# Kernel tuning notes

Measured on AMD Instinct MI355X. Metric: run time of the kernel, lower is better.

Reference implementation:

```python
import jax, jax.numpy as jnp
import numpy as np

N = 4096          # num_nodes
B = 16            # num_graphs (equal-sized contiguous segments)
L = 2             # max degree -> (L+1)**2 = 9 spherical components
NUM_DEG = (L + 1) ** 2
F = 128           # input feature dim
FQK = 128         # query/key feature dim
FV = 128          # value feature dim
MAX_FREQ = 8.0
MAX_LEN = 10.0

# degree index of each spherical component: [0, 1,1,1, 2,2,2,2,2]
DEG_IDX = np.array([l for l in range(L + 1) for _ in range(2 * l + 1)], dtype=np.int32)
# Lebedev grid num=6: octahedron vertices, equal weights 1/6
GRID_U = np.array([[1, 0, 0], [-1, 0, 0], [0, 1, 0], [0, -1, 0], [0, 0, 1], [0, 0, -1]], dtype=np.float32)
GRID_W = np.full((6,), 1.0 / 6.0, dtype=np.float32)


def _edense(x, W, b, deg_idx):
    y = jnp.einsum('npmf,mfg->npmg', x, W[deg_idx])
    return y.at[:, :, 0, :].add(b)


def _erope(x, cos, sin):
    # x: (N, 1, M9, Fqk); cos/sin: (N, G, H) with H = Fqk // 2
    x1 = x[:, None, :, :, 0::2]  # (N,1,1,M9,H) -> broadcast over G
    x2 = x[:, None, :, :, 1::2]
    c = cos[:, :, None, None, :]
    s = sin[:, :, None, None, :]
    r1 = x1 * c - x2 * s
    r2 = x1 * s + x2 * c
    out = jnp.stack([r1, r2], axis=-1)  # interleave pairs back
    return out.reshape(out.shape[:-2] + (-1,))  # (N, G, 1, M9, Fqk)


def setup_inputs() -> dict:
    key = jax.random.key(0)
    ks = jax.random.split(key, 8)
    inputs = jax.random.normal(ks[0], (N, 1, NUM_DEG, F), jnp.float32)
    positions = jax.random.normal(ks[1], (N, 3), jnp.float32) * 3.0
    # contiguous equal-sized graph segments (jraph-style padding convention)
    batch_segments = jnp.repeat(jnp.arange(B), N // B)
    graph_mask = jnp.ones((B,), bool)
    s = 1.0 / np.sqrt(F)
    Wq = jax.random.normal(ks[2], (L + 1, F, FQK), jnp.float32) * s
    Wk = jax.random.normal(ks[3], (L + 1, F, FQK), jnp.float32) * s
    Wv = jax.random.normal(ks[4], (L + 1, F, FV), jnp.float32) * s
    bq = jnp.zeros((FQK,), jnp.float32)
    bk = jnp.zeros((FQK,), jnp.float32)
    bv = jnp.zeros((FV,), jnp.float32)
    return dict(inputs=inputs, positions=positions, batch_segments=batch_segments,
                graph_mask=graph_mask, Wq=Wq, bq=bq, Wk=Wk, bk=bk, Wv=Wv, bv=bv)


def reference(inputs, positions, batch_segments, graph_mask, Wq, bq, Wk, bk, Wv, bv):
    deg_idx = jnp.asarray(DEG_IDX)
    grid_u = jnp.asarray(GRID_U)
    grid_w = jnp.asarray(GRID_W)
    G = grid_u.shape[0]
    # frequencies per frequency_init_fn: linspace(0, max_freq, Fqk/2) / max_length
    theta = jnp.linspace(0.0, MAX_FREQ, FQK // 2, dtype=jnp.float32) / MAX_LEN  # (H,)

    q = _edense(inputs, Wq, bq, deg_idx)  # (N,1,M9,FQK)
    k = _edense(inputs, Wk, bk, deg_idx)
    v = _edense(inputs, Wv, bv, deg_idx)  # (N,1,M9,FV)

    # Euclidean RoPE phases: angle[n,g,h] = (pos_n . u_g) * theta_h
    phase = positions @ grid_u.T           # (N,G)
    ang = phase[:, :, None] * theta        # (N,G,H)
    cos, sin = jnp.cos(ang), jnp.sin(ang)

    Mdim = NUM_DEG * FQK
    Ddim = NUM_DEG * FV
    qr = _erope(q, cos, sin).reshape(N, G, Mdim)  # (N,G,M)
    kr = _erope(k, cos, sin).reshape(N, G, Mdim)
    vf = v.reshape(N, Ddim)

    # per-graph linear attention with Lebedev quadrature (contiguous equal segments)
    n = N // B
    qr_b = qr.reshape(B, n, G, Mdim)
    kr_b = kr.reshape(B, n, G, Mdim)
    v_b = vf.reshape(B, n, Ddim)
    kv = jnp.einsum('bngm,bnd->bgmd', kr_b, v_b)          # KV summaries
    kv = kv * grid_w[None, :, None, None]                 # quadrature weights
    out = jnp.einsum('bngm,bgmd->bnd', qr_b, kv)          # integrate over grid
    out = out.reshape(N, 1, NUM_DEG, FV)
    mask = graph_mask[batch_segments]                     # (N,)
    return jnp.where(mask[:, None, None, None], out, 0.0)
```

## Files before the change

### kernel.cpp

```cpp
#include <hip/hip_runtime.h>


typedef unsigned short u16;
typedef __attribute__((ext_vector_type(8))) short short8;
typedef __attribute__((ext_vector_type(4))) float f32x4;

static constexpr int N_NODES = 4096;
static constexpr int NBATCH  = 16;
static constexpr int NB      = 256;
static constexpr int NDEG    = 9;
static constexpr int MD      = NDEG * 128;
static constexpr int KTOT    = 6 * MD;
static constexpr size_t ASLICE = (size_t)NBATCH * NB * NB;

static constexpr size_t OFF_WT  = 0;
static constexpr size_t OFF_QR  = OFF_WT  + (size_t)9*16384*2;
static constexpr size_t OFF_KR  = OFF_QR  + (size_t)N_NODES*KTOT*2;
static constexpr size_t OFF_VT  = OFF_KR  + (size_t)N_NODES*KTOT*2;
static constexpr size_t OFF_AP  = OFF_VT  + (size_t)N_NODES*MD*2;

__device__ inline u16 f2bf(float x) {
    union { float f; unsigned u; } v; v.f = x;
    unsigned r = v.u + 0x7fffu + ((v.u >> 16) & 1u);
    return (u16)(r >> 16);
}
__device__ inline float bf2f(u16 h) {
    union { unsigned u; float f; } v; v.u = ((unsigned)h) << 16; return v.f;
}
__device__ inline unsigned pk2bf(float a, float b) {
#if __has_builtin(__builtin_amdgcn_cvt_pk_bf16_f32)
    typedef __attribute__((ext_vector_type(2))) __bf16 bf2_t;
    union { bf2_t v; unsigned u; } cv;
    cv.v = __builtin_amdgcn_cvt_pk_bf16_f32(a, b);
    return cv.u;
#else
    return (unsigned)f2bf(a) | ((unsigned)f2bf(b) << 16);
#endif
}

__global__ __launch_bounds__(256) void k_prep(const float* __restrict__ Wq,
                                              const float* __restrict__ Wk,
                                              const float* __restrict__ Wv,
                                              u16* __restrict__ wt) {
    int t = blockIdx.x, tid = threadIdx.x;
    int blk = t >> 2, tt = t & 3;
    int mat = blk / 3, l = blk % 3;
    const float* W = (mat == 0 ? Wq : (mat == 1 ? Wk : Wv)) + (size_t)l * 16384;
    int j0 = (tt >> 1) * 64, f0 = (tt & 1) * 64;
    __shared__ u16 tile[64 * 72];
    for (int e = tid; e < 1024; e += 256) {
        int r = e >> 4, c = e & 15;
        float4 wv = *(const float4*)(W + (size_t)(f0 + r) * 128 + j0 + c * 4);
        tile[(c * 4 + 0) * 72 + r] = f2bf(wv.x);
        tile[(c * 4 + 1) * 72 + r] = f2bf(wv.y);
        tile[(c * 4 + 2) * 72 + r] = f2bf(wv.z);
        tile[(c * 4 + 3) * 72 + r] = f2bf(wv.w);
    }
    __syncthreads();
    u16* dst = wt + (size_t)blk * 16384;
    for (int e = tid; e < 512; e += 256) {
        int j = e >> 3, c = e & 7;
        *(uint4*)(dst + (size_t)(j0 + j) * 128 + f0 + c * 8) = *(const uint4*)(tile + j * 72 + c * 8);
    }
}

__global__ __launch_bounds__(256) void k_qkv(const float* __restrict__ X,
                                             const u16* __restrict__ wt,
                                             const float* __restrict__ bq,
                                             const float* __restrict__ bk,
                                             const float* __restrict__ bv,
                                             const float* __restrict__ pos,
                                             u16* __restrict__ qr,
                                             u16* __restrict__ kr,
                                             u16* __restrict__ vt) {
    const int nt = blockIdx.x, m = blockIdx.y, mat = blockIdx.z;
    const int n0 = nt * 64;
    const int deg = (m == 0) ? 0 : (m < 4 ? 1 : 2);
    const int tid = threadIdx.x;

    __shared__ u16 smem[26112];
    __shared__ float posS[192];
    u16* Xs = smem;
    u16* Ws = smem + 64 * 136;

    if (tid < 192) posS[tid] = pos[(size_t)n0 * 3 + tid];

    for (int e = tid; e < 2048; e += 256) {
        int r = e >> 5, f4 = e & 31;
        float4 xv = *(const float4*)(X + (size_t)(n0 + r) * MD + m * 128 + f4 * 4);
        uint2 o = make_uint2(pk2bf(xv.x, xv.y), pk2bf(xv.z, xv.w));
        *(uint2*)(Xs + r * 136 + f4 * 4) = o;
    }
    {
        const uint4* wsrc = (const uint4*)(wt + (size_t)(mat * 3 + deg) * 16384);
        for (int e = tid; e < 2048; e += 256) {
            int j = e >> 4, f8 = e & 15;
            *(uint4*)(Ws + j * 136 + f8 * 8) = wsrc[j * 16 + f8];
        }
    }
    __syncthreads();

    const int w = tid >> 6, lane = tid & 63, quad = lane >> 4, lrow = lane & 15;
    f32x4 acc[8];
#pragma unroll
    for (int ct = 0; ct < 8; ct++) acc[ct] = (f32x4){0.f, 0.f, 0.f, 0.f};
#pragma unroll
    for (int ks = 0; ks < 4; ks++) {
        short8 a = *(const short8*)(Xs + (w * 16 + lrow) * 136 + ks * 32 + quad * 8);
#pragma unroll
        for (int ct = 0; ct < 8; ct++) {
            short8 bfr = *(const short8*)(Ws + (ct * 16 + lrow) * 136 + ks * 32 + quad * 8);
            acc[ct] = __builtin_amdgcn_mfma_f32_16x16x32_bf16(a, bfr, acc[ct], 0, 0, 0);
        }
    }

    const float* bias = (mat == 0) ? bq : ((mat == 1) ? bk : bv);
    float yv[8][4];
#pragma unroll
    for (int ct = 0; ct < 8; ct++) {
        float bj = (m == 0) ? bias[ct * 16 + lrow] : 0.0f;
#pragma unroll
        for (int r = 0; r < 4; r++) yv[ct][r] = acc[ct][r] + bj;
    }

    if (mat == 2) {
        u16* T = Ws;
        const int nlb = w * 16 + quad * 4;
        __syncthreads();
#pragma unroll
        for (int ct = 0; ct < 8; ct++) {
            int j = ct * 16 + lrow;
            *(unsigned*)(T + j * 66 + nlb)     = pk2bf(yv[ct][0], yv[ct][1]);
            *(unsigned*)(T + j * 66 + nlb + 2) = pk2bf(yv[ct][2], yv[ct][3]);
        }
        __syncthreads();
        for (int e = tid; e < 1024; e += 256) {
            int d = e >> 3, c = e & 7;
            *(uint4*)(vt + (size_t)(m * 128 + d) * N_NODES + n0 + c * 8) =
                *(const uint4*)(T + d * 66 + c * 8);
        }
        return;
    }

    float pv[8][4];
#pragma unroll
    for (int ct = 0; ct < 8; ct++)
#pragma unroll
        for (int r = 0; r < 4; r++) pv[ct][r] = __shfl_xor(yv[ct][r], 1);

    float pr[4][3];
#pragma unroll
    for (int r = 0; r < 4; r++) {
        int nl = w * 16 + quad * 4 + r;
#pragma unroll
        for (int gp = 0; gp < 3; gp++) pr[r][gp] = posS[nl * 3 + gp];
    }
    const float thq = (float)(lrow >> 1) * (8.0f / 630.0f);
    const float th8 = 8.0f * (8.0f / 630.0f);

    u16* O0 = Xs;
    u16* O1 = Ws;
    u16* dst = (mat == 0) ? qr : kr;
    const bool even = !(lrow & 1);

    for (int gp = 0; gp < 3; gp++) {
        __syncthreads();
#pragma unroll
        for (int ct = 0; ct < 8; ct++) {
            float th = thq + (float)ct * th8;
#pragma unroll
            for (int r = 0; r < 4; r++) {
                int nl = w * 16 + quad * 4 + r;
                float s, c;
                __sincosf(pr[r][gp] * th, &s, &c);
                float t1 = yv[ct][r] * c, t2 = pv[ct][r] * s;
                float r0, r1;
                if (even) { r0 = t1 - t2; r1 = t1 + t2; }
                else      { r0 = t1 + t2; r1 = t1 - t2; }
                O0[nl * 136 + ct * 16 + lrow] = f2bf(r0);
                O1[nl * 136 + ct * 16 + lrow] = f2bf(r1);
            }
        }
        __syncthreads();
        for (int e = tid; e < 1024; e += 256) {
            int nl = e >> 4, c = e & 15;
            size_t o0 = ((size_t)(gp * 2) * N_NODES + n0 + nl) * MD + m * 128 + c * 8;
            *(uint4*)(dst + o0)                      = *(const uint4*)(O0 + nl * 136 + c * 8);
            *(uint4*)(dst + o0 + (size_t)N_NODES*MD) = *(const uint4*)(O1 + nl * 136 + c * 8);
        }
    }
}

__global__ __launch_bounds__(256) void k_gemm1(const u16* __restrict__ qr,
                                               const u16* __restrict__ kr,
                                               u16* __restrict__ Apart) {
    int idx = blockIdx.x;
    int grp = idx >> 6;
    int sub = idx & 63;
    int c   = sub & 7;
    int j   = sub >> 3;
    int bg  = grp * 4 + (c & 3);
    int g   = bg >> 4, b = bg & 15;
    int tr  = (c >> 2) * 2 + (j & 1);
    int tc  = j >> 1;

    int qn0 = b * NB + tr * 64, kn0 = b * NB + tc * 64;
    const size_t gbase = (size_t)g * N_NODES;
    int tid = threadIdx.x;
    __shared__ u16 Qs[64 * 72];
    __shared__ u16 Ks[64 * 72];
    int w = tid >> 6, lane = tid & 63, quad = lane >> 4, lrow = lane & 15;

    f32x4 acc[4];
#pragma unroll
    for (int ct = 0; ct < 4; ct++) acc[ct] = (f32x4){0.f, 0.f, 0.f, 0.f};

    for (int kc = 0; kc < MD / 64; kc++) {
        int k0 = kc * 64;
#pragma unroll
        for (int e = tid; e < 512; e += 256) {
            int r = e >> 3, s = e & 7;
            *(uint4*)(Qs + r * 72 + s * 8) = *(const uint4*)(qr + (gbase + qn0 + r) * MD + k0 + s * 8);
            *(uint4*)(Ks + r * 72 + s * 8) = *(const uint4*)(kr + (gbase + kn0 + r) * MD + k0 + s * 8);
        }
        __syncthreads();
#pragma unroll
        for (int ks = 0; ks < 2; ks++) {
            short8 a = *(const short8*)(Qs + (w * 16 + lrow) * 72 + ks * 32 + quad * 8);
#pragma unroll
            for (int ct = 0; ct < 4; ct++) {
                short8 bfr = *(const short8*)(Ks + (ct * 16 + lrow) * 72 + ks * 32 + quad * 8);
                acc[ct] = __builtin_amdgcn_mfma_f32_16x16x32_bf16(a, bfr, acc[ct], 0, 0, 0);
            }
        }
        __syncthreads();
    }
    u16* dst = Apart + ((size_t)g * NBATCH + b) * (NB * NB);
#pragma unroll
    for (int ct = 0; ct < 4; ct++)
#pragma unroll
        for (int r = 0; r < 4; r++) {
            int rib = tr * 64 + w * 16 + quad * 4 + r;
            int cib = tc * 64 + ct * 16 + lrow;
            dst[(size_t)rib * NB + cib] = f2bf(acc[ct][r]);
        }
}

__global__ __launch_bounds__(256) void k_gemm2(const u16* __restrict__ Ap,
                                               const u16* __restrict__ vt,
                                               const int* __restrict__ gmask,
                                               float* __restrict__ out) {
    int idx = blockIdx.x;
    int c   = idx & 7;
    int u   = idx >> 3;
    int pr9 = u / 9;
    int dcb = u - pr9 * 9;
    int pair = pr9 * 8 + c;
    int rt  = pair >> 4, b = pair & 15;
    int d0 = dcb * 128;
    int tid = threadIdx.x;
    __shared__ u16 As[64 * 72];
    __shared__ u16 Vs[128 * 72];
    int w = tid >> 6, lane = tid & 63, quad = lane >> 4, lrow = lane & 15;

    f32x4 acc[8];
#pragma unroll
    for (int ct = 0; ct < 8; ct++) acc[ct] = (f32x4){0.f, 0.f, 0.f, 0.f};

    const float sc6 = 1.0f / 6.0f;
    for (int kc = 0; kc < 4; kc++) {
        int k0 = kc * 64;
#pragma unroll
        for (int e = tid; e < 512; e += 256) {
            int r = e >> 3, c8 = e & 7;
            size_t off = (size_t)b * (NB * NB) + (size_t)(rt * 64 + r) * NB + k0 + c8 * 8;
            float sacc[8];
#pragma unroll
            for (int i = 0; i < 8; i++) sacc[i] = 0.f;
#pragma unroll
            for (int s = 0; s < 6; s++) {
                uint4 v = *(const uint4*)(Ap + (size_t)s * ASLICE + off);
                const unsigned* uu = (const unsigned*)&v;
#pragma unroll
                for (int h = 0; h < 4; h++) {
                    sacc[h * 2]     += bf2f((u16)(uu[h] & 0xffff));
                    sacc[h * 2 + 1] += bf2f((u16)(uu[h] >> 16));
                }
            }
            unsigned o32[4];
#pragma unroll
            for (int i = 0; i < 4; i++) o32[i] = pk2bf(sacc[i * 2] * sc6, sacc[i * 2 + 1] * sc6);
            *(uint4*)(As + r * 72 + c8 * 8) = *(const uint4*)o32;
        }
#pragma unroll
        for (int e = tid; e < 1024; e += 256) {
            int rr = e >> 3, sc2 = e & 7;
            *(uint4*)(Vs + rr * 72 + sc2 * 8) =
                *(const uint4*)(vt + (size_t)(d0 + rr) * N_NODES + b * NB + k0 + sc2 * 8);
        }
        __syncthreads();
#pragma unroll
        for (int ks = 0; ks < 2; ks++) {
            short8 a = *(const short8*)(As + (w * 16 + lrow) * 72 + ks * 32 + quad * 8);
#pragma unroll
            for (int ct = 0; ct < 8; ct++) {
                short8 bfr = *(const short8*)(Vs + (ct * 16 + lrow) * 72 + ks * 32 + quad * 8);
                acc[ct] = __builtin_amdgcn_mfma_f32_16x16x32_bf16(a, bfr, acc[ct], 0, 0, 0);
            }
        }
        __syncthreads();
    }
    int mv = gmask[b];
#pragma unroll
    for (int ct = 0; ct < 8; ct++)
#pragma unroll
        for (int r = 0; r < 4; r++) {
            int node = b * NB + rt * 64 + w * 16 + quad * 4 + r;
            int d = d0 + ct * 16 + lrow;
            out[(size_t)node * MD + d] = mv ? acc[ct][r] : 0.0f;
        }
}

extern "C" void kernel_launch(void* const* d_in, const int* in_sizes, int n_in,
                              void* d_out, int out_size, void* d_ws, size_t ws_size,
                              hipStream_t stream) {
    (void)in_sizes; (void)n_in; (void)out_size; (void)ws_size;

    const float* X    = (const float*)d_in[0];
    const float* pos  = (const float*)d_in[1];
    const int*   gmask= (const int*)  d_in[3];
    const float* Wq   = (const float*)d_in[4];
    const float* bq   = (const float*)d_in[5];
    const float* Wk   = (const float*)d_in[6];
    const float* bk   = (const float*)d_in[7];
    const float* Wv   = (const float*)d_in[8];
    const float* bv   = (const float*)d_in[9];
    float* out = (float*)d_out;

    char* ws = (char*)d_ws;
    u16*   wt   = (u16*)  (ws + OFF_WT);
    u16*   qrp  = (u16*)  (ws + OFF_QR);
    u16*   krp  = (u16*)  (ws + OFF_KR);
    u16*   vtp  = (u16*)  (ws + OFF_VT);
    u16*   App  = (u16*)  (ws + OFF_AP);

    k_prep <<<dim3(36),         dim3(256), 0, stream>>>(Wq, Wk, Wv, wt);
    k_qkv  <<<dim3(64, 9, 3),   dim3(256), 0, stream>>>(X, wt, bq, bk, bv, pos, qrp, krp, vtp);
    k_gemm1<<<dim3(1536),       dim3(256), 0, stream>>>(qrp, krp, App);
    k_gemm2<<<dim3(576),        dim3(256), 0, stream>>>(App, vtp, gmask, out);
}
```

Measured before the change: 170.2 us.

## Precompute RoPE trig table, enlarge gemm1 tiles, split grid-sum into separate kernel

Adds a kernel that precomputes the cos/sin table per node, axis and frequency so k_qkv reads it instead of calling sincos per element. k_gemm1 now computes 128x128 output tiles per block instead of 64x64, raising reuse of loaded Q/K data and cutting the block count by four. The six-slice grid reduction moves out of k_gemm2 into a standalone k_asum kernel, which avoids repeating the reduction for every d-column block. The cost is two extra launches plus extra global traffic for the trig table and the reduced A matrix, and fewer, larger gemm1 blocks that leave less parallelism.

```diff
diff --git a/kernel.cpp b/kernel.cpp
--- a/kernel.cpp
+++ b/kernel.cpp
@@ -18,6 +18,8 @@
 static constexpr size_t OFF_KR  = OFF_QR  + (size_t)N_NODES*KTOT*2;
 static constexpr size_t OFF_VT  = OFF_KR  + (size_t)N_NODES*KTOT*2;
 static constexpr size_t OFF_AP  = OFF_VT  + (size_t)N_NODES*MD*2;
+static constexpr size_t OFF_TAB = OFF_AP;
+static constexpr size_t OFF_A2  = OFF_QR;
 
 __device__ inline u16 f2bf(float x) {
     union { float f; unsigned u; } v; v.f = x;
@@ -64,12 +66,24 @@
     }
 }
 
+__global__ __launch_bounds__(256) void k_trig(const float* __restrict__ pos,
+                                              float2* __restrict__ tab) {
+    int tid = threadIdx.x;
+    int n  = blockIdx.x * 4 + (tid >> 6);
+    int gp = blockIdx.y;
+    int i  = tid & 63;
+    float ang = pos[(size_t)n * 3 + gp] * ((float)i * (8.0f / 630.0f));
+    float s, c;
+    __sincosf(ang, &s, &c);
+    tab[((size_t)n * 3 + gp) * 64 + i] = make_float2(c, s);
+}
+
 __global__ __launch_bounds__(256) void k_qkv(const float* __restrict__ X,
                                              const u16* __restrict__ wt,
                                              const float* __restrict__ bq,
                                              const float* __restrict__ bk,
                                              const float* __restrict__ bv,
-                                             const float* __restrict__ pos,
+                                             const float2* __restrict__ tab,
                                              u16* __restrict__ qr,
                                              u16* __restrict__ kr,
                                              u16* __restrict__ vt) {
@@ -79,11 +93,8 @@
     const int tid = threadIdx.x;
 
     __shared__ u16 smem[26112];
-    __shared__ float posS[192];
     u16* Xs = smem;
     u16* Ws = smem + 64 * 136;
-
-    if (tid < 192) posS[tid] = pos[(size_t)n0 * 3 + tid];
 
     for (int e = tid; e < 2048; e += 256) {
         int r = e >> 5, f4 = e & 31;
@@ -148,16 +159,6 @@
 #pragma unroll
         for (int r = 0; r < 4; r++) pv[ct][r] = __shfl_xor(yv[ct][r], 1);
 
-    float pr[4][3];
-#pragma unroll
-    for (int r = 0; r < 4; r++) {
-        int nl = w * 16 + quad * 4 + r;
-#pragma unroll
-        for (int gp = 0; gp < 3; gp++) pr[r][gp] = posS[nl * 3 + gp];
-    }
-    const float thq = (float)(lrow >> 1) * (8.0f / 630.0f);
-    const float th8 = 8.0f * (8.0f / 630.0f);
-
     u16* O0 = Xs;
     u16* O1 = Ws;
     u16* dst = (mat == 0) ? qr : kr;
@@ -166,14 +167,13 @@
     for (int gp = 0; gp < 3; gp++) {
         __syncthreads();
 #pragma unroll
-        for (int ct = 0; ct < 8; ct++) {
-            float th = thq + (float)ct * th8;
-#pragma unroll
-            for (int r = 0; r < 4; r++) {
-                int nl = w * 16 + quad * 4 + r;
-                float s, c;
-                __sincosf(pr[r][gp] * th, &s, &c);
-                float t1 = yv[ct][r] * c, t2 = pv[ct][r] * s;
+        for (int r = 0; r < 4; r++) {
+            int nl = w * 16 + quad * 4 + r;
+            const float2* tn = tab + ((size_t)(n0 + nl) * 3 + gp) * 64 + (lrow >> 1);
+#pragma unroll
+            for (int ct = 0; ct < 8; ct++) {
+                float2 cs = tn[ct * 8];
+                float t1 = yv[ct][r] * cs.x, t2 = pv[ct][r] * cs.y;
                 float r0, r1;
                 if (even) { r0 = t1 - t2; r1 = t1 + t2; }
                 else      { r0 = t1 + t2; r1 = t1 - t2; }
@@ -195,30 +195,31 @@
                                                const u16* __restrict__ kr,
                                                u16* __restrict__ Apart) {
     int idx = blockIdx.x;
-    int grp = idx >> 6;
-    int sub = idx & 63;
-    int c   = sub & 7;
-    int j   = sub >> 3;
-    int bg  = grp * 4 + (c & 3);
+    int c   = idx & 7;
+    int u   = idx >> 3;
+    int p   = u >> 2;
+    int t   = u & 3;
+    int bg  = p * 8 + c;
     int g   = bg >> 4, b = bg & 15;
-    int tr  = (c >> 2) * 2 + (j & 1);
-    int tc  = j >> 1;
-
-    int qn0 = b * NB + tr * 64, kn0 = b * NB + tc * 64;
+    int tr  = t >> 1, tc = t & 1;
+
+    int qn0 = b * NB + tr * 128, kn0 = b * NB + tc * 128;
     const size_t gbase = (size_t)g * N_NODES;
     int tid = threadIdx.x;
-    __shared__ u16 Qs[64 * 72];
-    __shared__ u16 Ks[64 * 72];
+    __shared__ u16 Qs[128 * 72];
+    __shared__ u16 Ks[128 * 72];
     int w = tid >> 6, lane = tid & 63, quad = lane >> 4, lrow = lane & 15;
 
-    f32x4 acc[4];
-#pragma unroll
-    for (int ct = 0; ct < 4; ct++) acc[ct] = (f32x4){0.f, 0.f, 0.f, 0.f};
+    f32x4 acc[2][8];
+#pragma unroll
+    for (int at = 0; at < 2; at++)
+#pragma unroll
+        for (int ct = 0; ct < 8; ct++) acc[at][ct] = (f32x4){0.f, 0.f, 0.f, 0.f};
 
     for (int kc = 0; kc < MD / 64; kc++) {
         int k0 = kc * 64;
 #pragma unroll
-        for (int e = tid; e < 512; e += 256) {
+        for (int e = tid; e < 1024; e += 256) {
             int r = e >> 3, s = e & 7;
             *(uint4*)(Qs + r * 72 + s * 8) = *(const uint4*)(qr + (gbase + qn0 + r) * MD + k0 + s * 8);
             *(uint4*)(Ks + r * 72 + s * 8) = *(const uint4*)(kr + (gbase + kn0 + r) * MD + k0 + s * 8);
@@ -226,27 +227,54 @@
         __syncthreads();
 #pragma unroll
         for (int ks = 0; ks < 2; ks++) {
-            short8 a = *(const short8*)(Qs + (w * 16 + lrow) * 72 + ks * 32 + quad * 8);
-#pragma unroll
-            for (int ct = 0; ct < 4; ct++) {
+            short8 a0 = *(const short8*)(Qs + (w * 32 + lrow) * 72 + ks * 32 + quad * 8);
+            short8 a1 = *(const short8*)(Qs + (w * 32 + 16 + lrow) * 72 + ks * 32 + quad * 8);
+#pragma unroll
+            for (int ct = 0; ct < 8; ct++) {
                 short8 bfr = *(const short8*)(Ks + (ct * 16 + lrow) * 72 + ks * 32 + quad * 8);
-                acc[ct] = __builtin_amdgcn_mfma_f32_16x16x32_bf16(a, bfr, acc[ct], 0, 0, 0);
+                acc[0][ct] = __builtin_amdgcn_mfma_f32_16x16x32_bf16(a0, bfr, acc[0][ct], 0, 0, 0);
+                acc[1][ct] = __builtin_amdgcn_mfma_f32_16x16x32_bf16(a1, bfr, acc[1][ct], 0, 0, 0);
             }
         }
         __syncthreads();
     }
     u16* dst = Apart + ((size_t)g * NBATCH + b) * (NB * NB);
 #pragma unroll
-    for (int ct = 0; ct < 4; ct++)
-#pragma unroll
-        for (int r = 0; r < 4; r++) {
-            int rib = tr * 64 + w * 16 + quad * 4 + r;
-            int cib = tc * 64 + ct * 16 + lrow;
-            dst[(size_t)rib * NB + cib] = f2bf(acc[ct][r]);
-        }
-}
-
-__global__ __launch_bounds__(256) void k_gemm2(const u16* __restrict__ Ap,
+    for (int at = 0; at < 2; at++)
+#pragma unroll
+        for (int ct = 0; ct < 8; ct++)
+#pragma unroll
+            for (int r = 0; r < 4; r++) {
+                int rib = tr * 128 + w * 32 + at * 16 + quad * 4 + r;
+                int cib = tc * 128 + ct * 16 + lrow;
+                dst[(size_t)rib * NB + cib] = f2bf(acc[at][ct][r]);
+            }
+}
+
+__global__ __launch_bounds__(256) void k_asum(const u16* __restrict__ Ap,
+                                              u16* __restrict__ A2) {
+    size_t t = (size_t)blockIdx.x * 256 + threadIdx.x;
+    float sacc[8];
+#pragma unroll
+    for (int i = 0; i < 8; i++) sacc[i] = 0.f;
+#pragma unroll
+    for (int s = 0; s < 6; s++) {
+        uint4 v = *(const uint4*)(Ap + (size_t)s * ASLICE + t * 8);
+        const unsigned* uu = (const unsigned*)&v;
+#pragma unroll
+        for (int h = 0; h < 4; h++) {
+            sacc[h * 2]     += bf2f((u16)(uu[h] & 0xffff));
+            sacc[h * 2 + 1] += bf2f((u16)(uu[h] >> 16));
+        }
+    }
+    const float sc6 = 1.0f / 6.0f;
+    unsigned o32[4];
+#pragma unroll
+    for (int i = 0; i < 4; i++) o32[i] = pk2bf(sacc[i * 2] * sc6, sacc[i * 2 + 1] * sc6);
+    *(uint4*)(A2 + t * 8) = *(const uint4*)o32;
+}
+
+__global__ __launch_bounds__(256) void k_gemm2(const u16* __restrict__ A2,
                                                const u16* __restrict__ vt,
                                                const int* __restrict__ gmask,
                                                float* __restrict__ out) {
@@ -267,30 +295,13 @@
 #pragma unroll
     for (int ct = 0; ct < 8; ct++) acc[ct] = (f32x4){0.f, 0.f, 0.f, 0.f};
 
-    const float sc6 = 1.0f / 6.0f;
     for (int kc = 0; kc < 4; kc++) {
         int k0 = kc * 64;
 #pragma unroll
         for (int e = tid; e < 512; e += 256) {
             int r = e >> 3, c8 = e & 7;
-            size_t off = (size_t)b * (NB * NB) + (size_t)(rt * 64 + r) * NB + k0 + c8 * 8;
-            float sacc[8];
-#pragma unroll
-            for (int i = 0; i < 8; i++) sacc[i] = 0.f;
-#pragma unroll
-            for (int s = 0; s < 6; s++) {
-                uint4 v = *(const uint4*)(Ap + (size_t)s * ASLICE + off);
-                const unsigned* uu = (const unsigned*)&v;
-#pragma unroll
-                for (int h = 0; h < 4; h++) {
-                    sacc[h * 2]     += bf2f((u16)(uu[h] & 0xffff));
-                    sacc[h * 2 + 1] += bf2f((u16)(uu[h] >> 16));
-                }
-            }
-            unsigned o32[4];
-#pragma unroll
-            for (int i = 0; i < 4; i++) o32[i] = pk2bf(sacc[i * 2] * sc6, sacc[i * 2 + 1] * sc6);
-            *(uint4*)(As + r * 72 + c8 * 8) = *(const uint4*)o32;
+            *(uint4*)(As + r * 72 + c8 * 8) =
+                *(const uint4*)(A2 + (size_t)b * (NB * NB) + (size_t)(rt * 64 + r) * NB + k0 + c8 * 8);
         }
 #pragma unroll
         for (int e = tid; e < 1024; e += 256) {
@@ -338,14 +349,18 @@
     float* out = (float*)d_out;
 
     char* ws = (char*)d_ws;
-    u16*   wt   = (u16*)  (ws + OFF_WT);
-    u16*   qrp  = (u16*)  (ws + OFF_QR);
-    u16*   krp  = (u16*)  (ws + OFF_KR);
-    u16*   vtp  = (u16*)  (ws + OFF_VT);
-    u16*   App  = (u16*)  (ws + OFF_AP);
+    u16*    wt   = (u16*)   (ws + OFF_WT);
+    u16*    qrp  = (u16*)   (ws + OFF_QR);
+    u16*    krp  = (u16*)   (ws + OFF_KR);
+    u16*    vtp  = (u16*)   (ws + OFF_VT);
+    u16*    App  = (u16*)   (ws + OFF_AP);
+    float2* tabp = (float2*)(ws + OFF_TAB);
+    u16*    a2p  = (u16*)   (ws + OFF_A2);
 
     k_prep <<<dim3(36),         dim3(256), 0, stream>>>(Wq, Wk, Wv, wt);
-    k_qkv  <<<dim3(64, 9, 3),   dim3(256), 0, stream>>>(X, wt, bq, bk, bv, pos, qrp, krp, vtp);
-    k_gemm1<<<dim3(1536),       dim3(256), 0, stream>>>(qrp, krp, App);
-    k_gemm2<<<dim3(576),        dim3(256), 0, stream>>>(App, vtp, gmask, out);
-}
+    k_trig <<<dim3(1024, 3),    dim3(256), 0, stream>>>(pos, tabp);
+    k_qkv  <<<dim3(64, 9, 3),   dim3(256), 0, stream>>>(X, wt, bq, bk, bv, tabp, qrp, krp, vtp);
+    k_gemm1<<<dim3(384),        dim3(256), 0, stream>>>(qrp, krp, App);
+    k_asum <<<dim3(512),        dim3(256), 0, stream>>>(App, a2p);
+    k_gemm2<<<dim3(576),        dim3(256), 0, stream>>>(a2p, vtp, gmask, out);
+}
```

Result: slower. 182.8 us (+7.4%).
